# Kernel optimization log

Hardware: AMD Instinct MI355X
Metric: run time of the kernel (lower is better)

The kernel has to match this reference:

```python
import jax, jax.numpy as jnp
import numpy as np
from functools import partial

_EPS = 1e-5

def _build_R_to_F():
    R_to_F = np.zeros((9, 16), dtype=np.float32)
    F_nonzero = [
        [(0, 0, 1.0), (1, 1, 1.0), (2, 2, 1.0)], [(1, 2, 1.0), (2, 1, -1.0)],
        [(2, 0, 1.0), (0, 2, -1.0)], [(0, 1, 1.0), (1, 0, -1.0)],
        [(1, 2, 1.0), (2, 1, -1.0)], [(0, 0, 1.0), (1, 1, -1.0), (2, 2, -1.0)],
        [(0, 1, 1.0), (1, 0, 1.0)], [(0, 2, 1.0), (2, 0, 1.0)],
        [(2, 0, 1.0), (0, 2, -1.0)], [(0, 1, 1.0), (1, 0, 1.0)],
        [(0, 0, -1.0), (1, 1, 1.0), (2, 2, -1.0)], [(1, 2, 1.0), (2, 1, 1.0)],
        [(0, 1, 1.0), (1, 0, -1.0)], [(0, 2, 1.0), (2, 0, 1.0)],
        [(1, 2, 1.0), (2, 1, 1.0)], [(0, 0, -1.0), (1, 1, -1.0), (2, 2, 1.0)],
    ]
    for F_ij, nonzero in enumerate(F_nonzero):
        for R_i, R_j, sign in nonzero:
            R_to_F[R_i * 3 + R_j, F_ij] = sign
    return jnp.asarray(R_to_F)

_R_TO_F = _build_R_to_F()

def _eig_leading(F, num_iterations=50):
    # F: (..., 4, 4) symmetric. Power iteration for the MOST POSITIVE eigenvalue.
    # Shift spectrum by Frobenius norm (upper bound on spectral radius) so the
    # most positive eigenvalue is also largest in magnitude.
    shift = jnp.sqrt(jnp.sum(F * F, axis=(-2, -1), keepdims=True))  # (...,1,1)
    F_shift = F + shift * jnp.eye(4, dtype=F.dtype)
    v0 = jnp.full(F.shape[:-1], 0.5, dtype=F.dtype)  # (...,4), unit norm

    def body(_, v):
        w = jnp.einsum('...ij,...j->...i', F_shift, v)
        return w / (jnp.linalg.norm(w, axis=-1, keepdims=True) + 1e-12)

    v = jax.lax.fori_loop(0, num_iterations, body, v0)
    eig = jnp.einsum('...i,...ij,...j->...', v, F, v)  # Rayleigh quotient (unit v)
    return eig, v

def reference(X_mobile, X_target, method_iter=50):
    # X_mobile: (S, A, 3), X_target: (T, A, 3)
    num_atoms = X_mobile.shape[1]
    Xm = X_mobile - X_mobile.mean(axis=1, keepdims=True)
    Xt = X_target - X_target.mean(axis=1, keepdims=True)
    # Cross-covariance: (S, T, 3, 3)
    R = jnp.einsum('sai,taj->stij', Xm, Xt)
    S, T = R.shape[0], R.shape[1]
    F = (R.reshape(S, T, 9) @ _R_TO_F).reshape(S, T, 4, 4)
    top_eig, _ = _eig_leading(F, num_iterations=method_iter)  # (S, T)
    norms = (Xm ** 2).sum(axis=(-1, -2))[:, None] + (Xt ** 2).sum(axis=(-1, -2))[None, :]
    sqRMSD = jax.nn.relu((norms - 2.0 * top_eig) / (num_atoms + _EPS))
    return jnp.sqrt(sqRMSD)

def setup_inputs() -> dict:
    key = jax.random.key(0)
    k1, k2 = jax.random.split(key)
    X_mobile = jax.random.normal(k1, (2048, 128, 3), dtype=jnp.float32)
    X_target = jax.random.normal(k2, (2048, 128, 3), dtype=jnp.float32)
    return {"X_mobile": X_mobile, "X_target": X_target}
```

## Files before the change

### kernel.cpp

```cpp
#include <hip/hip_runtime.h>
#include <math.h>

#define NS 2048
#define NT 2048
#define NATOMS 128

typedef __attribute__((ext_vector_type(8))) short bf16x8;
typedef __attribute__((ext_vector_type(4))) float f32x4;

static __device__ __forceinline__ unsigned short f2bf(float f) {
    unsigned int u = __float_as_uint(f);
    unsigned int r = (u + 0x7fffu + ((u >> 16) & 1u)) >> 16;
    return (unsigned short)r;
}
static __device__ __forceinline__ float bf2f(unsigned short h) {
    return __uint_as_float(((unsigned int)h) << 16);
}

__global__ __launch_bounds__(64) void center_bf16_kernel(
    const float* __restrict__ X, unsigned short* __restrict__ Hi,
    unsigned short* __restrict__ Lo, float* __restrict__ norms)
{
    const int s = blockIdx.x;
    const int lane = threadIdx.x;
    const float* xs = X + (size_t)s * (NATOMS * 3);
    float x0 = xs[lane * 3 + 0];
    float y0 = xs[lane * 3 + 1];
    float z0 = xs[lane * 3 + 2];
    float x1 = xs[(lane + 64) * 3 + 0];
    float y1 = xs[(lane + 64) * 3 + 1];
    float z1 = xs[(lane + 64) * 3 + 2];
    float sx = x0 + x1, sy = y0 + y1, sz = z0 + z1;
#pragma unroll
    for (int off = 32; off > 0; off >>= 1) {
        sx += __shfl_xor(sx, off);
        sy += __shfl_xor(sy, off);
        sz += __shfl_xor(sz, off);
    }
    const float inv_n = 1.0f / (float)NATOMS;
    const float mx = sx * inv_n, my = sy * inv_n, mz = sz * inv_n;
    x0 -= mx; y0 -= my; z0 -= mz;
    x1 -= mx; y1 -= my; z1 -= mz;

    const size_t base = (size_t)s * 384;
    const float v[3][2] = {{x0, x1}, {y0, y1}, {z0, z1}};
#pragma unroll
    for (int c = 0; c < 3; ++c)
#pragma unroll
        for (int h = 0; h < 2; ++h) {
            const unsigned short hb = f2bf(v[c][h]);
            const unsigned short lb = f2bf(v[c][h] - bf2f(hb));
            Hi[base + c * 128 + h * 64 + lane] = hb;
            Lo[base + c * 128 + h * 64 + lane] = lb;
        }

    float nsq = x0 * x0 + y0 * y0 + z0 * z0 + x1 * x1 + y1 * y1 + z1 * z1;
#pragma unroll
    for (int off = 32; off > 0; off >>= 1) nsq += __shfl_xor(nsq, off);
    if (lane == 0) norms[s] = nsq;
}

__global__ __launch_bounds__(256, 6) void pair_mfma_kernel(
    const unsigned short* __restrict__ Ahi, const unsigned short* __restrict__ Alo,
    const unsigned short* __restrict__ Bhi, const unsigned short* __restrict__ Blo,
    const float* __restrict__ norm_s, const float* __restrict__ norm_t,
    float* __restrict__ out)
{
    const int tid = threadIdx.x;
    const int wave = tid >> 6;
    const int lane = tid & 63;
    const int nrow = lane & 15;
    const int kgrp = lane >> 4;
    const int sBase = blockIdx.x * 16;
    const int tBase = blockIdx.y * 64 + wave * 16;

    const unsigned aOff = (unsigned)((sBase + nrow) * 384 + kgrp * 8);
    const unsigned bOff = (unsigned)((tBase + nrow) * 384 + kgrp * 8);

    f32x4 acc[3][3];
#pragma unroll
    for (int i = 0; i < 3; ++i)
#pragma unroll
        for (int j = 0; j < 3; ++j) acc[i][j] = (f32x4){0.f, 0.f, 0.f, 0.f};

#pragma unroll 1
    for (int ks = 0; ks < 4; ++ks) {
        const unsigned ak = aOff + ks * 32;
        const unsigned bk = bOff + ks * 32;
        {
            bf16x8 ah[3], bh[3];
#pragma unroll
            for (int c = 0; c < 3; ++c) {
                ah[c] = *reinterpret_cast<const bf16x8*>(Ahi + ak + c * 128);
                bh[c] = *reinterpret_cast<const bf16x8*>(Bhi + bk + c * 128);
            }
#pragma unroll
            for (int i = 0; i < 3; ++i)
#pragma unroll
                for (int j = 0; j < 3; ++j)
                    acc[i][j] = __builtin_amdgcn_mfma_f32_16x16x32_bf16(
                        ah[i], bh[j], acc[i][j], 0, 0, 0);
            __builtin_amdgcn_sched_barrier(0);
            bf16x8 bl[3];
#pragma unroll
            for (int c = 0; c < 3; ++c)
                bl[c] = *reinterpret_cast<const bf16x8*>(Blo + bk + c * 128);
#pragma unroll
            for (int i = 0; i < 3; ++i)
#pragma unroll
                for (int j = 0; j < 3; ++j)
                    acc[i][j] = __builtin_amdgcn_mfma_f32_16x16x32_bf16(
                        ah[i], bl[j], acc[i][j], 0, 0, 0);
            __builtin_amdgcn_sched_barrier(0);
        }
        {
            bf16x8 al[3], bh2[3];
            unsigned bkL = bk;
            asm volatile("" : "+v"(bkL));
#pragma unroll
            for (int c = 0; c < 3; ++c) {
                al[c]  = *reinterpret_cast<const bf16x8*>(Alo + ak + c * 128);
                bh2[c] = *reinterpret_cast<const bf16x8*>(Bhi + bkL + c * 128);
            }
#pragma unroll
            for (int i = 0; i < 3; ++i)
#pragma unroll
                for (int j = 0; j < 3; ++j)
                    acc[i][j] = __builtin_amdgcn_mfma_f32_16x16x32_bf16(
                        al[i], bh2[j], acc[i][j], 0, 0, 0);
            __builtin_amdgcn_sched_barrier(0);
        }
    }

    float D0[4], D1[4], D2[4], D3[4];
    float E01[4], E02[4], E03[4], E12[4], E13[4], E23[4];
    float q0[4], q1[4], q2[4], q3[4];
#pragma unroll
    for (int u = 0; u < 4; ++u) {
        const float Sxx = acc[0][0][u], Sxy = acc[0][1][u], Sxz = acc[0][2][u];
        const float Syx = acc[1][0][u], Syy = acc[1][1][u], Syz = acc[1][2][u];
        const float Szx = acc[2][0][u], Szy = acc[2][1][u], Szz = acc[2][2][u];
        const float F00 =  Sxx + Syy + Szz;
        const float F11 =  Sxx - Syy - Szz;
        const float F22 = -Sxx + Syy - Szz;
        const float F33 = -Sxx - Syy + Szz;
        const float F01 = Syz - Szy;
        const float F02 = Szx - Sxz;
        const float F03 = Sxy - Syx;
        const float F12 = Sxy + Syx;
        const float F13 = Sxz + Szx;
        const float F23 = Syz + Szy;
        const float fro = sqrtf(F00 * F00 + F11 * F11 + F22 * F22 + F33 * F33 +
                                2.0f * (F01 * F01 + F02 * F02 + F03 * F03 +
                                        F12 * F12 + F13 * F13 + F23 * F23));
        D0[u] = F00 + fro;
        D1[u] = F11 + fro;
        D2[u] = F22 + fro;
        D3[u] = F33 + fro;
        E01[u] = F01; E02[u] = F02; E03[u] = F03;
        E12[u] = F12; E13[u] = F13; E23[u] = F23;
        q0[u] = 0.5f; q1[u] = 0.5f; q2[u] = 0.5f; q3[u] = 0.5f;
    }

    for (int blk = 0; blk < 10; ++blk) {
#pragma unroll
        for (int k = 0; k < 5; ++k) {
#pragma unroll
            for (int u = 0; u < 4; ++u) {
                const float w0 = fmaf(E03[u], q3[u], fmaf(E02[u], q2[u],
                                 fmaf(E01[u], q1[u], D0[u] * q0[u])));
                const float w1 = fmaf(E13[u], q3[u], fmaf(E12[u], q2[u],
                                 fmaf(D1[u], q1[u], E01[u] * q0[u])));
                const float w2 = fmaf(E23[u], q3[u], fmaf(D2[u], q2[u],
                                 fmaf(E12[u], q1[u], E02[u] * q0[u])));
                const float w3 = fmaf(D3[u], q3[u], fmaf(E23[u], q2[u],
                                 fmaf(E13[u], q1[u], E03[u] * q0[u])));
                q0[u] = w0; q1[u] = w1; q2[u] = w2; q3[u] = w3;
            }
        }
#pragma unroll
        for (int u = 0; u < 4; ++u) {
            const float a0 = q0[u], a1 = q1[u], a2 = q2[u], a3 = q3[u];
            const float nn = a0 * a0 + a1 * a1 + a2 * a2 + a3 * a3;
            const float sc = __builtin_amdgcn_rsqf(nn);
            q0[u] = a0 * sc; q1[u] = a1 * sc;
            q2[u] = a2 * sc; q3[u] = a3 * sc;
        }
    }

    const float inv_na = 1.0f / (128.0f + 1e-5f);
    const float Gb = norm_t[tBase + nrow];
#pragma unroll
    for (int u = 0; u < 4; ++u) {
        const int srow = sBase + kgrp * 4 + u;
        const float Ga = norm_s[srow];
        const float a0 = q0[u], a1 = q1[u], a2 = q2[u], a3 = q3[u];
        const float fro = (((D0[u] + D1[u]) + D2[u]) + D3[u]) * 0.25f;
        const float m0 = D0[u] * a0 + E01[u] * a1 + E02[u] * a2 + E03[u] * a3;
        const float m1 = E01[u] * a0 + D1[u] * a1 + E12[u] * a2 + E13[u] * a3;
        const float m2 = E02[u] * a0 + E12[u] * a1 + D2[u] * a2 + E23[u] * a3;
        const float m3 = E03[u] * a0 + E13[u] * a1 + E23[u] * a2 + D3[u] * a3;
        const float num = a0 * m0 + a1 * m1 + a2 * m2 + a3 * m3;
        const float den = a0 * a0 + a1 * a1 + a2 * a2 + a3 * a3;
        const float eig = num * __builtin_amdgcn_rcpf(den) - fro;
        float sq = (Ga + Gb - 2.0f * eig) * inv_na;
        out[(size_t)srow * NT + tBase + nrow] = sqrtf(fmaxf(sq, 0.0f));
    }
}

extern "C" void kernel_launch(void* const* d_in, const int* in_sizes, int n_in,
                              void* d_out, int out_size, void* d_ws, size_t ws_size,
                              hipStream_t stream) {
    const float* Xm = (const float*)d_in[0];
    const float* Xt = (const float*)d_in[1];
    float* out = (float*)d_out;

    unsigned short* ws16 = (unsigned short*)d_ws;
    unsigned short* Ahi = ws16;
    unsigned short* Alo = Ahi + (size_t)NS * 384;
    unsigned short* Bhi = Alo + (size_t)NS * 384;
    unsigned short* Blo = Bhi + (size_t)NT * 384;
    float* norm_m = (float*)(Blo + (size_t)NT * 384);
    float* norm_t = norm_m + NS;

    center_bf16_kernel<<<NS, 64, 0, stream>>>(Xm, Ahi, Alo, norm_m);
    center_bf16_kernel<<<NT, 64, 0, stream>>>(Xt, Bhi, Blo, norm_t);

    dim3 grid(NS / 16, NT / 64);
    pair_mfma_kernel<<<grid, 256, 0, stream>>>(Ahi, Alo, Bhi, Blo,
                                               norm_m, norm_t, out);
}
```

Before: 146.5 us.

## Split power-iteration epilogue into two passes and drop occupancy hint and sched barriers

The per-lane power iteration over four output rows now runs in two sequential groups of two rows each. This cuts the live register set in the epilogue but halves the independent FMA chains available to hide latency. The min-waves-per-EU launch-bound hint is removed and the sched_barrier fences between MFMA groups are dropped, so the compiler can choose register allocation and interleave loads with MFMAs freely. The risk is lower ILP in the serial iteration chain and a possible change in occupancy.

```diff
diff --git a/kernel.cpp b/kernel.cpp
--- a/kernel.cpp
+++ b/kernel.cpp
@@ -60,7 +60,7 @@
     if (lane == 0) norms[s] = nsq;
 }
 
-__global__ __launch_bounds__(256, 6) void pair_mfma_kernel(
+__global__ __launch_bounds__(256) void pair_mfma_kernel(
     const unsigned short* __restrict__ Ahi, const unsigned short* __restrict__ Alo,
     const unsigned short* __restrict__ Bhi, const unsigned short* __restrict__ Blo,
     const float* __restrict__ norm_s, const float* __restrict__ norm_t,
@@ -100,7 +100,6 @@
                 for (int j = 0; j < 3; ++j)
                     acc[i][j] = __builtin_amdgcn_mfma_f32_16x16x32_bf16(
                         ah[i], bh[j], acc[i][j], 0, 0, 0);
-            __builtin_amdgcn_sched_barrier(0);
             bf16x8 bl[3];
 #pragma unroll
             for (int c = 0; c < 3; ++c)
@@ -111,7 +110,6 @@
                 for (int j = 0; j < 3; ++j)
                     acc[i][j] = __builtin_amdgcn_mfma_f32_16x16x32_bf16(
                         ah[i], bl[j], acc[i][j], 0, 0, 0);
-            __builtin_amdgcn_sched_barrier(0);
         }
         {
             bf16x8 al[3], bh2[3];
@@ -128,83 +126,88 @@
                 for (int j = 0; j < 3; ++j)
                     acc[i][j] = __builtin_amdgcn_mfma_f32_16x16x32_bf16(
                         al[i], bh2[j], acc[i][j], 0, 0, 0);
-            __builtin_amdgcn_sched_barrier(0);
-        }
-    }
-
-    float D0[4], D1[4], D2[4], D3[4];
-    float E01[4], E02[4], E03[4], E12[4], E13[4], E23[4];
-    float q0[4], q1[4], q2[4], q3[4];
-#pragma unroll
-    for (int u = 0; u < 4; ++u) {
-        const float Sxx = acc[0][0][u], Sxy = acc[0][1][u], Sxz = acc[0][2][u];
-        const float Syx = acc[1][0][u], Syy = acc[1][1][u], Syz = acc[1][2][u];
-        const float Szx = acc[2][0][u], Szy = acc[2][1][u], Szz = acc[2][2][u];
-        const float F00 =  Sxx + Syy + Szz;
-        const float F11 =  Sxx - Syy - Szz;
-        const float F22 = -Sxx + Syy - Szz;
-        const float F33 = -Sxx - Syy + Szz;
-        const float F01 = Syz - Szy;
-        const float F02 = Szx - Sxz;
-        const float F03 = Sxy - Syx;
-        const float F12 = Sxy + Syx;
-        const float F13 = Sxz + Szx;
-        const float F23 = Syz + Szy;
-        const float fro = sqrtf(F00 * F00 + F11 * F11 + F22 * F22 + F33 * F33 +
-                                2.0f * (F01 * F01 + F02 * F02 + F03 * F03 +
-                                        F12 * F12 + F13 * F13 + F23 * F23));
-        D0[u] = F00 + fro;
-        D1[u] = F11 + fro;
-        D2[u] = F22 + fro;
-        D3[u] = F33 + fro;
-        E01[u] = F01; E02[u] = F02; E03[u] = F03;
-        E12[u] = F12; E13[u] = F13; E23[u] = F23;
-        q0[u] = 0.5f; q1[u] = 0.5f; q2[u] = 0.5f; q3[u] = 0.5f;
-    }
-
-    for (int blk = 0; blk < 10; ++blk) {
-#pragma unroll
-        for (int k = 0; k < 5; ++k) {
-#pragma unroll
-            for (int u = 0; u < 4; ++u) {
-                const float w0 = fmaf(E03[u], q3[u], fmaf(E02[u], q2[u],
-                                 fmaf(E01[u], q1[u], D0[u] * q0[u])));
-                const float w1 = fmaf(E13[u], q3[u], fmaf(E12[u], q2[u],
-                                 fmaf(D1[u], q1[u], E01[u] * q0[u])));
-                const float w2 = fmaf(E23[u], q3[u], fmaf(D2[u], q2[u],
-                                 fmaf(E12[u], q1[u], E02[u] * q0[u])));
-                const float w3 = fmaf(D3[u], q3[u], fmaf(E23[u], q2[u],
-                                 fmaf(E13[u], q1[u], E03[u] * q0[u])));
-                q0[u] = w0; q1[u] = w1; q2[u] = w2; q3[u] = w3;
-            }
-        }
-#pragma unroll
-        for (int u = 0; u < 4; ++u) {
-            const float a0 = q0[u], a1 = q1[u], a2 = q2[u], a3 = q3[u];
-            const float nn = a0 * a0 + a1 * a1 + a2 * a2 + a3 * a3;
-            const float sc = __builtin_amdgcn_rsqf(nn);
-            q0[u] = a0 * sc; q1[u] = a1 * sc;
-            q2[u] = a2 * sc; q3[u] = a3 * sc;
         }
     }
 
     const float inv_na = 1.0f / (128.0f + 1e-5f);
     const float Gb = norm_t[tBase + nrow];
-#pragma unroll
-    for (int u = 0; u < 4; ++u) {
-        const int srow = sBase + kgrp * 4 + u;
-        const float Ga = norm_s[srow];
-        const float a0 = q0[u], a1 = q1[u], a2 = q2[u], a3 = q3[u];
-        const float fro = (((D0[u] + D1[u]) + D2[u]) + D3[u]) * 0.25f;
-        const float m0 = D0[u] * a0 + E01[u] * a1 + E02[u] * a2 + E03[u] * a3;
-        const float m1 = E01[u] * a0 + D1[u] * a1 + E12[u] * a2 + E13[u] * a3;
-        const float m2 = E02[u] * a0 + E12[u] * a1 + D2[u] * a2 + E23[u] * a3;
-        const float m3 = E03[u] * a0 + E13[u] * a1 + E23[u] * a2 + D3[u] * a3;
-        const float num = a0 * m0 + a1 * m1 + a2 * m2 + a3 * m3;
-        const float den = a0 * a0 + a1 * a1 + a2 * a2 + a3 * a3;
-        const float eig = num * __builtin_amdgcn_rcpf(den) - fro;
-        float sq = (Ga + Gb - 2.0f * eig) * inv_na;
-        out[(size_t)srow * NT + tBase + nrow] = sqrtf(fmaxf(sq, 0.0f));
+
+#pragma unroll 1
+    for (int g = 0; g < 2; ++g) {
+        float D0[2], D1[2], D2[2], D3[2];
+        float E01[2], E02[2], E03[2], E12[2], E13[2], E23[2];
+        float q0[2], q1[2], q2[2], q3[2];
+#pragma unroll
+        for (int j = 0; j < 2; ++j) {
+            const int u = g * 2 + j;
+            const float Sxx = acc[0][0][u], Sxy = acc[0][1][u], Sxz = acc[0][2][u];
+            const float Syx = acc[1][0][u], Syy = acc[1][1][u], Syz = acc[1][2][u];
+            const float Szx = acc[2][0][u], Szy = acc[2][1][u], Szz = acc[2][2][u];
+            const float F00 =  Sxx + Syy + Szz;
+            const float F11 =  Sxx - Syy - Szz;
+            const float F22 = -Sxx + Syy - Szz;
+            const float F33 = -Sxx - Syy + Szz;
+            const float F01 = Syz - Szy;
+            const float F02 = Szx - Sxz;
+            const float F03 = Sxy - Syx;
+            const float F12 = Sxy + Syx;
+            const float F13 = Sxz + Szx;
+            const float F23 = Syz + Szy;
+            const float fro = sqrtf(F00 * F00 + F11 * F11 + F22 * F22 + F33 * F33 +
+                                    2.0f * (F01 * F01 + F02 * F02 + F03 * F03 +
+                                            F12 * F12 + F13 * F13 + F23 * F23));
+            D0[j] = F00 + fro;
+            D1[j] = F11 + fro;
+            D2[j] = F22 + fro;
+            D3[j] = F33 + fro;
+            E01[j] = F01; E02[j] = F02; E03[j] = F03;
+            E12[j] = F12; E13[j] = F13; E23[j] = F23;
+            q0[j] = 0.5f; q1[j] = 0.5f; q2[j] = 0.5f; q3[j] = 0.5f;
+        }
+
+        for (int blk = 0; blk < 10; ++blk) {
+#pragma unroll
+            for (int k = 0; k < 5; ++k) {
+#pragma unroll
+                for (int j = 0; j < 2; ++j) {
+                    const float w0 = fmaf(E03[j], q3[j], fmaf(E02[j], q2[j],
+                                     fmaf(E01[j], q1[j], D0[j] * q0[j])));
+                    const float w1 = fmaf(E13[j], q3[j], fmaf(E12[j], q2[j],
+                                     fmaf(D1[j], q1[j], E01[j] * q0[j])));
+                    const float w2 = fmaf(E23[j], q3[j], fmaf(D2[j], q2[j],
+                                     fmaf(E12[j], q1[j], E02[j] * q0[j])));
+                    const float w3 = fmaf(D3[j], q3[j], fmaf(E23[j], q2[j],
+                                     fmaf(E13[j], q1[j], E03[j] * q0[j])));
+                    q0[j] = w0; q1[j] = w1; q2[j] = w2; q3[j] = w3;
+                }
+            }
+#pragma unroll
+            for (int j = 0; j < 2; ++j) {
+                const float a0 = q0[j], a1 = q1[j], a2 = q2[j], a3 = q3[j];
+                const float nn = a0 * a0 + a1 * a1 + a2 * a2 + a3 * a3;
+                const float sc = __builtin_amdgcn_rsqf(nn);
+                q0[j] = a0 * sc; q1[j] = a1 * sc;
+                q2[j] = a2 * sc; q3[j] = a3 * sc;
+            }
+        }
+
+#pragma unroll
+        for (int j = 0; j < 2; ++j) {
+            const int u = g * 2 + j;
+            const int srow = sBase + kgrp * 4 + u;
+            const float Ga = norm_s[srow];
+            const float a0 = q0[j], a1 = q1[j], a2 = q2[j], a3 = q3[j];
+            const float fro = (((D0[j] + D1[j]) + D2[j]) + D3[j]) * 0.25f;
+            const float m0 = D0[j] * a0 + E01[j] * a1 + E02[j] * a2 + E03[j] * a3;
+            const float m1 = E01[j] * a0 + D1[j] * a1 + E12[j] * a2 + E13[j] * a3;
+            const float m2 = E02[j] * a0 + E12[j] * a1 + D2[j] * a2 + E23[j] * a3;
+            const float m3 = E03[j] * a0 + E13[j] * a1 + E23[j] * a2 + D3[j] * a3;
+            const float num = a0 * m0 + a1 * m1 + a2 * m2 + a3 * m3;
+            const float den = a0 * a0 + a1 * a1 + a2 * a2 + a3 * a3;
+            const float eig = num * __builtin_amdgcn_rcpf(den) - fro;
+            float sq = (Ga + Gb - 2.0f * eig) * inv_na;
+            out[(size_t)srow * NT + tBase + nrow] = sqrtf(fmaxf(sq, 0.0f));
+        }
     }
 }
 
```

Result: slower. 156.4 us (+6.8%).
